# Optimization experiments

Hardware: AMD Instinct MI355X
Metric: run time of the kernel (lower is better)

The kernel has to match this reference:

```python
import jax, jax.numpy as jnp
import numpy as np

T, H_IN = 2048, 84
HID = 256
NA = 18


def _conv(x, w, b, stride):
    # x: [N,C,H,W], w: [O,I,kh,kw]
    y = jax.lax.conv_general_dilated(
        x, w, window_strides=(stride, stride), padding='VALID',
        dimension_numbers=('NCHW', 'OIHW', 'NCHW'))
    return jax.nn.relu(y + b[None, :, None, None])


def setup_inputs() -> dict:
    key = jax.random.key(0)
    ks = jax.random.split(key, 17)
    p = lambda k, shape, s=0.05: (jax.random.normal(k, shape, jnp.float32) * s)
    return {
        'input_frames': jax.random.uniform(ks[0], (T, 1, H_IN, H_IN), jnp.float32),
        'conv1_w': p(ks[1], (32, 1, 8, 8)),   'conv1_b': p(ks[2], (32,)),
        'conv2_w': p(ks[3], (64, 32, 4, 4)),  'conv2_b': p(ks[4], (64,)),
        'conv3_w': p(ks[5], (256, 64, 3, 3)), 'conv3_b': p(ks[6], (256,)),
        'attn_w1': p(ks[7], (HID, HID)),      'attn_b1': p(ks[8], (HID,)),
        'attn_w2': p(ks[9], (HID, HID)),      'attn_b2': p(ks[10], (HID,)),
        'lstm_w_ih': p(ks[11], (4 * HID, HID)), 'lstm_w_hh': p(ks[12], (4 * HID, HID)),
        'lstm_b_ih': p(ks[13], (4 * HID,)),     'lstm_b_hh': p(ks[14], (4 * HID,)),
        'q_w': p(ks[15], (NA, HID)),          'q_b': p(ks[16], (NA,)),
    }


def reference(input_frames, conv1_w, conv1_b, conv2_w, conv2_b, conv3_w, conv3_b,
              attn_w1, attn_b1, attn_w2, attn_b2,
              lstm_w_ih, lstm_w_hh, lstm_b_ih, lstm_b_hh, q_w, q_b):
    # CNN over all frames at once (loop in torch was over frames; math identical)
    x = _conv(input_frames, conv1_w, conv1_b, 4)   # [T,32,20,20]
    x = _conv(x, conv2_w, conv2_b, 2)              # [T,64,9,9]
    fm = _conv(x, conv3_w, conv3_b, 1)             # [T,256,7,7]
    t, c, hh, ww = fm.shape
    # build_vector: vectors[i, ch] = fm[ch, y, x], i = y*W + x
    vecs = fm.reshape(t, c, hh * ww).transpose(0, 2, 1)  # [T,49,256]

    def step(carry, v):
        h, cc = carry  # [256], [256]
        # additive attention; softmax over the 256 feature dim per spatial vector
        s = jnp.tanh(v @ attn_w1.T + attn_b1 + h)              # [49,256]
        w = jax.nn.softmax(s @ attn_w2.T + attn_b2, axis=-1)   # [49,256]
        ctx = jnp.sum(w * v, axis=0)                           # [256]
        # single-layer LSTM cell, torch gate order i,f,g,o
        gates = ctx @ lstm_w_ih.T + lstm_b_ih + h @ lstm_w_hh.T + lstm_b_hh
        i, f, g, o = jnp.split(gates, 4)
        c_new = jax.nn.sigmoid(f) * cc + jax.nn.sigmoid(i) * jnp.tanh(g)
        h_new = jax.nn.sigmoid(o) * jnp.tanh(c_new)
        return (h_new, c_new), None

    h0 = jnp.zeros((HID,), fm.dtype)
    (h_T, _), _ = jax.lax.scan(step, (h0, h0), vecs)
    q = h_T @ q_w.T + q_b          # [18]
    return q[None, :]              # [1, nr_actions], matches torch output
```

## Files before the change

kernel.cpp:

```cpp
#include <hip/hip_runtime.h>
#include <hip/hip_bf16.h>
#include <math.h>


#define T_FRAMES 2048
#define NI 49
#define HID 256
#define NA 18
#define NWG 8

typedef __bf16 v8bf __attribute__((ext_vector_type(8)));
typedef float v4f __attribute__((ext_vector_type(4)));

static constexpr size_t OFF_FM1   = 0;
static constexpr size_t OFF_FM2   = 104857600;
static constexpr size_t OFF_VECS  = 147324928;
static constexpr size_t OFF_W2B   = 250085376;
static constexpr size_t OFF_WIHB  = OFF_W2B  + 131072;
static constexpr size_t OFF_WHHB  = OFF_WIHB + 524288;
static constexpr size_t OFF_W1T   = OFF_WHHB + 524288;
static constexpr size_t OFF_HBUF  = OFF_FM2;
static constexpr size_t OFF_CPUB  = OFF_FM2 + 1024;
static constexpr size_t OFF_FLH   = OFF_FM2 + 9216;
static constexpr size_t OFF_FLC   = OFF_FM2 + 10240;

__global__ void prep_weights(const float* __restrict__ w2, const float* __restrict__ wih,
                             const float* __restrict__ whh, const float* __restrict__ w1,
                             __bf16* w2b, __bf16* wihb, __bf16* whhb, float* w1t) {
  int idx = blockIdx.x * 256 + threadIdx.x;
  int stride = gridDim.x * 256;
  for (int i = idx; i < 65536; i += stride) w2b[i] = (__bf16)w2[i];
  for (int i = idx; i < 262144; i += stride) wihb[i] = (__bf16)wih[i];
  for (int i = idx; i < 262144; i += stride) whhb[i] = (__bf16)whh[i];
  for (int i = idx; i < 65536; i += stride) {
    int r = i >> 8, c = i & 255;
    w1t[c * 256 + r] = w1[i];
  }
}

__global__ void conv1_k(const float* __restrict__ x, const float* __restrict__ w,
                        const float* __restrict__ b, float* __restrict__ y) {
  int idx = blockIdx.x * 256 + threadIdx.x;
  if (idx >= T_FRAMES * 32 * 20 * 20) return;
  int xx = idx % 20, yy = (idx / 20) % 20, o = (idx / 400) % 32, t = idx / 12800;
  const float* xp = x + t * 7056 + yy * 4 * 84 + xx * 4;
  const float* wp = w + o * 64;
  float acc = b[o];
  #pragma unroll
  for (int ky = 0; ky < 8; ky++)
    #pragma unroll
    for (int kx = 0; kx < 8; kx++)
      acc += xp[ky * 84 + kx] * wp[ky * 8 + kx];
  y[idx] = fmaxf(acc, 0.f);
}

__global__ __launch_bounds__(256) void conv2_k(const float* __restrict__ fm1, const float* __restrict__ w,
                                               const float* __restrict__ b, float* __restrict__ fm2) {
  __shared__ float xs[32 * 400];
  int t = blockIdx.x, tid = threadIdx.x;
  for (int i = tid; i < 12800; i += 256) xs[i] = fm1[t * 12800 + i];
  __syncthreads();
  int o = tid >> 2, q = tid & 3;
  int p0 = q * 21, p1 = (p0 + 21 < 81) ? p0 + 21 : 81;
  int ob[21];
  #pragma unroll
  for (int i2 = 0; i2 < 21; i2++) {
    int p = p0 + i2; if (p > 80) p = 80;
    int yy = p / 9, xx2 = p - yy * 9;
    ob[i2] = yy * 40 + xx2 * 2;
  }
  float acc[21];
  #pragma unroll
  for (int i2 = 0; i2 < 21; i2++) acc[i2] = 0.f;
  for (int c = 0; c < 32; c++) {
    int cbase = c * 400;
    for (int ky = 0; ky < 4; ky++)
      for (int kx = 0; kx < 4; kx++) {
        float wgt = w[((o * 32 + c) * 4 + ky) * 4 + kx];
        int kyo = ky * 20 + kx;
        #pragma unroll
        for (int i2 = 0; i2 < 21; i2++)
          acc[i2] += wgt * xs[cbase + ob[i2] + kyo];
      }
  }
  float bo = b[o];
  #pragma unroll
  for (int i2 = 0; i2 < 21; i2++) {
    int p = p0 + i2;
    if (p < p1) fm2[t * 5184 + o * 81 + p] = fmaxf(acc[i2] + bo, 0.f);
  }
}

__global__ __launch_bounds__(256) void conv3_k(const float* __restrict__ fm2, const float* __restrict__ w,
                                               const float* __restrict__ b, float* __restrict__ vecs) {
  __shared__ float xs[64 * 81];
  __shared__ float ws4[256][37];
  int t = blockIdx.x, tid = threadIdx.x;
  for (int i = tid; i < 64 * 81; i += 256) xs[i] = fm2[t * 5184 + i];
  float acc[49];
  #pragma unroll
  for (int i = 0; i < 49; i++) acc[i] = 0.f;
  for (int c0 = 0; c0 < 64; c0 += 4) {
    __syncthreads();
    for (int i = tid; i < 256 * 36; i += 256) {
      int oo = i / 36, j = i - oo * 36;
      ws4[oo][j] = w[oo * 576 + c0 * 9 + j];
    }
    __syncthreads();
    for (int cc = 0; cc < 4; cc++)
      for (int ky = 0; ky < 3; ky++)
        for (int kx = 0; kx < 3; kx++) {
          float wgt = ws4[tid][cc * 9 + ky * 3 + kx];
          const float* xp = &xs[(c0 + cc) * 81 + ky * 9 + kx];
          #pragma unroll
          for (int yy = 0; yy < 7; yy++)
            #pragma unroll
            for (int xx = 0; xx < 7; xx++)
              acc[yy * 7 + xx] += wgt * xp[yy * 9 + xx];
        }
  }
  float bo = b[tid];
  for (int i = 0; i < 49; i++)
    vecs[(t * 49 + i) * 256 + tid] = fmaxf(acc[i] + bo, 0.f);
}

__global__ __launch_bounds__(256) void aprep_k(const float* __restrict__ vecs, const float* __restrict__ w1t,
                                               const float* __restrict__ b1, float* __restrict__ A) {
  __shared__ float vs[49][256];
  int t = blockIdx.x, tid = threadIdx.x;
  for (int i = tid; i < 49 * 256; i += 256) vs[i >> 8][i & 255] = vecs[t * 12544 + i];
  __syncthreads();
  float acc[49];
  #pragma unroll
  for (int i = 0; i < 49; i++) acc[i] = 0.f;
  for (int k = 0; k < 256; k++) {
    float wgt = w1t[k * 256 + tid];
    #pragma unroll
    for (int i = 0; i < 49; i++) acc[i] += vs[i][k] * wgt;
  }
  float bb = b1[tid];
  for (int i = 0; i < 49; i++) A[(t * 49 + i) * 256 + tid] = acc[i] + bb;
}

__global__ void init_comm(unsigned* flh, unsigned* flc) {
  int idx = blockIdx.x * 512 + threadIdx.x;
  if (idx < NWG * 32) { flh[idx] = 0u; flc[idx] = 0u; }
}

__device__ __forceinline__ float tanh_fast(float x) {
  float e = __expf(2.f * x);
  return 1.f - 2.f / (e + 1.f);
}

__global__ __launch_bounds__(256, 1) void scan_k(
    const float* __restrict__ A, const float* __restrict__ vecs,
    const __bf16* __restrict__ w2b, const __bf16* __restrict__ wihb, const __bf16* __restrict__ whhb,
    const float* __restrict__ b2g, const float* __restrict__ bihg, const float* __restrict__ bhhg,
    const float* __restrict__ qw, const float* __restrict__ qb,
    float* hbuf, unsigned* cpub, unsigned* flh, unsigned* flc, float* out) {
  __shared__ __bf16 Ss[16][264];
  __shared__ float hs[HID];
  __shared__ __bf16 hbf[HID];
  __shared__ float Wt[8][HID];
  __shared__ float cxp[8][HID];
  __shared__ float b2s[HID];
  __shared__ float gb[4][32];

  const int w = blockIdx.x;
  const int tid = threadIdx.x;
  const int lane = tid & 63;
  const int wv = tid >> 6;
  const int quad = lane >> 4;
  const int l15 = lane & 15;
  const int r0 = 6 * w;
  const int nr = (w < 7) ? 6 : 7;
  const int prow = tid >> 5;
  const int pcol = (tid & 31) * 8;

  for (int i = tid; i < 16 * 264; i += 256) (&Ss[0][0])[i] = (__bf16)0.f;
  for (int i = tid; i < 8 * HID; i += 256) (&cxp[0][0])[i] = 0.f;
  b2s[tid] = b2g[tid];
  hs[tid] = 0.f;
  hbf[tid] = (__bf16)0.f;
  float cbias[4];
  if (tid < 32) {
    #pragma unroll
    for (int g = 0; g < 4; g++) {
      int row = 256 * g + 32 * w + tid;
      cbias[g] = bihg[row] + bhhg[row];
    }
  }
  float creg = 0.f;

  v8bf BW2[4][8];
  #pragma unroll
  for (int ntl = 0; ntl < 4; ntl++) {
    const int row = wv * 64 + ntl * 16 + l15;
    #pragma unroll
    for (int k = 0; k < 8; k++)
      BW2[ntl][k] = *(const v8bf*)(w2b + row * 256 + k * 32 + quad * 8);
  }
  v8bf BIH[2][8], BHH[2][8];
  #pragma unroll
  for (int nt = 0; nt < 2; nt++) {
    const int row = 256 * wv + 32 * w + nt * 16 + l15;
    #pragma unroll
    for (int k = 0; k < 8; k++) {
      BIH[nt][k] = *(const v8bf*)(wihb + row * 256 + k * 32 + quad * 8);
      BHH[nt][k] = *(const v8bf*)(whhb + row * 256 + k * 32 + quad * 8);
    }
  }
  __syncthreads();

  for (int t = 0; t < T_FRAMES; t++) {
    int rr = r0 + prow; if (rr > 48) rr = 48;
    const float* Ap = A + ((long)t * NI + rr) * HID + pcol;
    const float* Vp = vecs + ((long)t * NI + rr) * HID + pcol;
    const float4 a40 = *(const float4*)(Ap);
    const float4 a41 = *(const float4*)(Ap + 4);
    const float4 v40 = *(const float4*)(Vp);
    const float4 v41 = *(const float4*)(Vp + 4);

    if (t > 0) {
      if (wv == 0) {
        const unsigned tgt = (unsigned)t;
        int guard = 0;
        while (true) {
          unsigned fv = (lane < NWG)
              ? __hip_atomic_load(&flh[lane * 32], __ATOMIC_RELAXED, __HIP_MEMORY_SCOPE_AGENT)
              : tgt;
          if (__all(fv >= tgt) || ++guard > 5000000) break;
          __builtin_amdgcn_s_sleep(1);
        }
      }
      __syncthreads();
      float hv = __hip_atomic_load(&hbuf[tid], __ATOMIC_RELAXED, __HIP_MEMORY_SCOPE_AGENT);
      hs[tid] = hv;
      hbf[tid] = (__bf16)hv;
      __syncthreads();
    }

    if (prow < nr) {
      const float* hp = &hs[pcol];
      v8bf sv;
      sv[0] = (__bf16)tanh_fast(a40.x + hp[0]);
      sv[1] = (__bf16)tanh_fast(a40.y + hp[1]);
      sv[2] = (__bf16)tanh_fast(a40.z + hp[2]);
      sv[3] = (__bf16)tanh_fast(a40.w + hp[3]);
      sv[4] = (__bf16)tanh_fast(a41.x + hp[4]);
      sv[5] = (__bf16)tanh_fast(a41.y + hp[5]);
      sv[6] = (__bf16)tanh_fast(a41.z + hp[6]);
      sv[7] = (__bf16)tanh_fast(a41.w + hp[7]);
      *(v8bf*)&Ss[prow][pcol] = sv;
    }
    __syncthreads();

    v4f acc[4];
    #pragma unroll
    for (int ntl = 0; ntl < 4; ntl++) acc[ntl] = (v4f){0.f, 0.f, 0.f, 0.f};
    #pragma unroll
    for (int k = 0; k < 8; k++) {
      const v8bf av = *(const v8bf*)&Ss[l15][k * 32 + quad * 8];
      #pragma unroll
      for (int ntl = 0; ntl < 4; ntl++)
        acc[ntl] = __builtin_amdgcn_mfma_f32_16x16x32_bf16(av, BW2[ntl][k], acc[ntl], 0, 0, 0);
    }
    if (quad < 2) {
      #pragma unroll
      for (int ntl = 0; ntl < 4; ntl++) {
        const int col = wv * 64 + ntl * 16 + l15;
        const float bb = b2s[col];
        #pragma unroll
        for (int reg = 0; reg < 4; reg++)
          Wt[quad * 4 + reg][col] = acc[ntl][reg] + bb;
      }
    }
    __syncthreads();

    if (prow < nr) {
      float x[8];
      *(float4*)&x[0] = *(const float4*)&Wt[prow][pcol];
      *(float4*)&x[4] = *(const float4*)&Wt[prow][pcol + 4];
      float m = x[0];
      #pragma unroll
      for (int i = 1; i < 8; i++) m = fmaxf(m, x[i]);
      #pragma unroll
      for (int off = 16; off; off >>= 1) m = fmaxf(m, __shfl_xor(m, off, 64));
      float e[8], sm = 0.f;
      #pragma unroll
      for (int i = 0; i < 8; i++) { e[i] = __expf(x[i] - m); sm += e[i]; }
      #pragma unroll
      for (int off = 16; off; off >>= 1) sm += __shfl_xor(sm, off, 64);
      const float inv = 1.f / sm;
      cxp[prow][pcol + 0] = e[0] * inv * v40.x;
      cxp[prow][pcol + 1] = e[1] * inv * v40.y;
      cxp[prow][pcol + 2] = e[2] * inv * v40.z;
      cxp[prow][pcol + 3] = e[3] * inv * v40.w;
      cxp[prow][pcol + 4] = e[4] * inv * v41.x;
      cxp[prow][pcol + 5] = e[5] * inv * v41.y;
      cxp[prow][pcol + 6] = e[6] * inv * v41.z;
      cxp[prow][pcol + 7] = e[7] * inv * v41.w;
    }
    __syncthreads();

    float cp = 0.f;
    #pragma unroll
    for (int r = 0; r < 8; r++) cp += cxp[r][tid];
    float cpo = __shfl_xor(cp, 1, 64);
    if ((tid & 1) == 0) {
      union { __bf16 b; unsigned short s; } lo, hi;
      lo.b = (__bf16)cp; hi.b = (__bf16)cpo;
      unsigned u = ((unsigned)hi.s << 16) | (unsigned)lo.s;
      __hip_atomic_store(&cpub[w * 256 + (tid >> 1)], u, __ATOMIC_RELAXED, __HIP_MEMORY_SCOPE_AGENT);
    }
    __syncthreads();
    if (tid == 0)
      __hip_atomic_store(&flc[w * 32], (unsigned)(t + 1), __ATOMIC_RELEASE, __HIP_MEMORY_SCOPE_AGENT);

    v4f gacc[2];
    gacc[0] = (v4f){0.f, 0.f, 0.f, 0.f};
    gacc[1] = (v4f){0.f, 0.f, 0.f, 0.f};
    #pragma unroll
    for (int k = 0; k < 8; k++) {
      v8bf hf;
      #pragma unroll
      for (int z = 0; z < 8; z++) hf[z] = (__bf16)0.f;
      if (l15 == 0) hf = *(const v8bf*)&hbf[k * 32 + quad * 8];
      gacc[0] = __builtin_amdgcn_mfma_f32_16x16x32_bf16(hf, BHH[0][k], gacc[0], 0, 0, 0);
      gacc[1] = __builtin_amdgcn_mfma_f32_16x16x32_bf16(hf, BHH[1][k], gacc[1], 0, 0, 0);
    }

    {
      const unsigned tgt = (unsigned)(t + 1);
      int guard = 0;
      while (true) {
        unsigned fv = (lane < NWG)
            ? __hip_atomic_load(&flc[lane * 32], __ATOMIC_RELAXED, __HIP_MEMORY_SCOPE_AGENT)
            : tgt;
        if (__all(fv >= tgt) || ++guard > 5000000) break;
        __builtin_amdgcn_s_sleep(1);
      }
    }

    #pragma unroll
    for (int k = 0; k < 8; k++) {
      union { unsigned long long u[2]; v8bf v; } pf;
      pf.u[0] = 0ull; pf.u[1] = 0ull;
      if (l15 < NWG) {
        const unsigned long long* src =
            (const unsigned long long*)(cpub + l15 * 256) + (k * 8 + quad * 2);
        pf.u[0] = __hip_atomic_load(src, __ATOMIC_RELAXED, __HIP_MEMORY_SCOPE_AGENT);
        pf.u[1] = __hip_atomic_load(src + 1, __ATOMIC_RELAXED, __HIP_MEMORY_SCOPE_AGENT);
      }
      gacc[0] = __builtin_amdgcn_mfma_f32_16x16x32_bf16(pf.v, BIH[0][k], gacc[0], 0, 0, 0);
      gacc[1] = __builtin_amdgcn_mfma_f32_16x16x32_bf16(pf.v, BIH[1][k], gacc[1], 0, 0, 0);
    }
    #pragma unroll
    for (int nt = 0; nt < 2; nt++) {
      float tot = gacc[nt][0] + gacc[nt][1] + gacc[nt][2] + gacc[nt][3];
      tot += __shfl_xor(tot, 16, 64);
      tot += __shfl_xor(tot, 32, 64);
      if (lane < 16) gb[wv][nt * 16 + lane] = tot;
    }
    __syncthreads();

    if (tid < 32) {
      float gi = gb[0][tid] + cbias[0];
      float gf = gb[1][tid] + cbias[1];
      float gg = gb[2][tid] + cbias[2];
      float go = gb[3][tid] + cbias[3];
      float si = 1.f / (1.f + __expf(-gi));
      float sf = 1.f / (1.f + __expf(-gf));
      float so = 1.f / (1.f + __expf(-go));
      creg = sf * creg + si * tanh_fast(gg);
      float hn = so * tanh_fast(creg);
      __hip_atomic_store(&hbuf[32 * w + tid], hn, __ATOMIC_RELAXED, __HIP_MEMORY_SCOPE_AGENT);
    }
    __syncthreads();
    if (tid == 0)
      __hip_atomic_store(&flh[w * 32], (unsigned)(t + 1), __ATOMIC_RELEASE, __HIP_MEMORY_SCOPE_AGENT);
  }

  if (w == 0) {
    if (wv == 0) {
      const unsigned tgt = (unsigned)T_FRAMES;
      int guard = 0;
      while (true) {
        unsigned fv = (lane < NWG)
            ? __hip_atomic_load(&flh[lane * 32], __ATOMIC_RELAXED, __HIP_MEMORY_SCOPE_AGENT)
            : tgt;
        if (__all(fv >= tgt) || ++guard > 5000000) break;
        __builtin_amdgcn_s_sleep(1);
      }
    }
    __syncthreads();
    hs[tid] = __hip_atomic_load(&hbuf[tid], __ATOMIC_RELAXED, __HIP_MEMORY_SCOPE_AGENT);
    __syncthreads();
    if (tid < NA) {
      float acc = qb[tid];
      for (int k = 0; k < HID; k++) acc += hs[k] * qw[tid * HID + k];
      out[tid] = acc;
    }
  }
}

extern "C" void kernel_launch(void* const* d_in, const int* in_sizes, int n_in,
                              void* d_out, int out_size, void* d_ws, size_t ws_size,
                              hipStream_t stream) {
  const float* frames = (const float*)d_in[0];
  const float* c1w = (const float*)d_in[1];
  const float* c1b = (const float*)d_in[2];
  const float* c2w = (const float*)d_in[3];
  const float* c2b = (const float*)d_in[4];
  const float* c3w = (const float*)d_in[5];
  const float* c3b = (const float*)d_in[6];
  const float* aw1 = (const float*)d_in[7];
  const float* ab1 = (const float*)d_in[8];
  const float* aw2 = (const float*)d_in[9];
  const float* ab2 = (const float*)d_in[10];
  const float* wih = (const float*)d_in[11];
  const float* whh = (const float*)d_in[12];
  const float* bih = (const float*)d_in[13];
  const float* bhh = (const float*)d_in[14];
  const float* qw  = (const float*)d_in[15];
  const float* qb  = (const float*)d_in[16];

  char* ws = (char*)d_ws;
  float*  fm1   = (float*)(ws + OFF_FM1);
  float*  A     = (float*)(ws + OFF_FM1);
  float*  fm2   = (float*)(ws + OFF_FM2);
  float*  vecs  = (float*)(ws + OFF_VECS);
  __bf16* w2b   = (__bf16*)(ws + OFF_W2B);
  __bf16* wihb  = (__bf16*)(ws + OFF_WIHB);
  __bf16* whhb  = (__bf16*)(ws + OFF_WHHB);
  float*  w1t   = (float*)(ws + OFF_W1T);
  float*    hbuf = (float*)(ws + OFF_HBUF);
  unsigned* cpub = (unsigned*)(ws + OFF_CPUB);
  unsigned* flh  = (unsigned*)(ws + OFF_FLH);
  unsigned* flc  = (unsigned*)(ws + OFF_FLC);

  prep_weights<<<256, 256, 0, stream>>>(aw2, wih, whh, aw1, w2b, wihb, whhb, w1t);
  conv1_k<<<102400, 256, 0, stream>>>(frames, c1w, c1b, fm1);
  conv2_k<<<T_FRAMES, 256, 0, stream>>>(fm1, c2w, c2b, fm2);
  conv3_k<<<T_FRAMES, 256, 0, stream>>>(fm2, c3w, c3b, vecs);
  aprep_k<<<T_FRAMES, 256, 0, stream>>>(vecs, w1t, ab1, A);
  init_comm<<<1, 512, 0, stream>>>(flh, flc);
  scan_k<<<NWG, 256, 0, stream>>>(A, vecs, w2b, wihb, whhb, ab2, bih, bhh, qw, qb,
                                  hbuf, cpub, flh, flc, (float*)d_out);
}
```

Baseline: 16.00 ms.

## Replace flag-based cross-workgroup sync with sequence-tagged 64-bit data packets

Each published h value and context pair is packed together with its step counter into one 64-bit word. Consumers poll the data itself until every tag matches, instead of waiting on separate release/acquire flags and then loading. This removes the flag stores, the extra __syncthreads around publishing, and a serial flag-then-data round trip on every LSTM step. In exchange every thread polls several words (32 per lane for the context), which adds L2 traffic and spin pressure, and the poll loop drops the s_sleep backoff.

```diff
diff --git a/kernel.cpp b/kernel.cpp
--- a/kernel.cpp
+++ b/kernel.cpp
@@ -8,9 +8,11 @@
 #define HID 256
 #define NA 18
 #define NWG 8
+#define POLL_MAX 1000000
 
 typedef __bf16 v8bf __attribute__((ext_vector_type(8)));
 typedef float v4f __attribute__((ext_vector_type(4)));
+typedef unsigned long long u64;
 
 static constexpr size_t OFF_FM1   = 0;
 static constexpr size_t OFF_FM2   = 104857600;
@@ -19,10 +21,15 @@
 static constexpr size_t OFF_WIHB  = OFF_W2B  + 131072;
 static constexpr size_t OFF_WHHB  = OFF_WIHB + 524288;
 static constexpr size_t OFF_W1T   = OFF_WHHB + 524288;
-static constexpr size_t OFF_HBUF  = OFF_FM2;
-static constexpr size_t OFF_CPUB  = OFF_FM2 + 1024;
-static constexpr size_t OFF_FLH   = OFF_FM2 + 9216;
-static constexpr size_t OFF_FLC   = OFF_FM2 + 10240;
+static constexpr size_t OFF_HPUB  = OFF_FM2;
+static constexpr size_t OFF_CPUB  = OFF_FM2 + 2048;
+
+__device__ __forceinline__ u64 ld_pair(const u64* p) {
+  return __hip_atomic_load(p, __ATOMIC_RELAXED, __HIP_MEMORY_SCOPE_AGENT);
+}
+__device__ __forceinline__ void st_pair(u64* p, u64 v) {
+  __hip_atomic_store(p, v, __ATOMIC_RELAXED, __HIP_MEMORY_SCOPE_AGENT);
+}
 
 __global__ void prep_weights(const float* __restrict__ w2, const float* __restrict__ wih,
                              const float* __restrict__ whh, const float* __restrict__ w1,
@@ -142,9 +149,10 @@
   for (int i = 0; i < 49; i++) A[(t * 49 + i) * 256 + tid] = acc[i] + bb;
 }
 
-__global__ void init_comm(unsigned* flh, unsigned* flc) {
-  int idx = blockIdx.x * 512 + threadIdx.x;
-  if (idx < NWG * 32) { flh[idx] = 0u; flc[idx] = 0u; }
+__global__ void init_comm(u64* hpub, u64* cpub) {
+  int idx = blockIdx.x * 256 + threadIdx.x;
+  if (idx < 256) hpub[idx] = 0ull;
+  if (idx < NWG * 128) cpub[idx] = 0ull;
 }
 
 __device__ __forceinline__ float tanh_fast(float x) {
@@ -157,14 +165,14 @@
     const __bf16* __restrict__ w2b, const __bf16* __restrict__ wihb, const __bf16* __restrict__ whhb,
     const float* __restrict__ b2g, const float* __restrict__ bihg, const float* __restrict__ bhhg,
     const float* __restrict__ qw, const float* __restrict__ qb,
-    float* hbuf, unsigned* cpub, unsigned* flh, unsigned* flc, float* out) {
+    u64* hpub, u64* cpub, float* out) {
   __shared__ __bf16 Ss[16][264];
-  __shared__ float hs[HID];
   __shared__ __bf16 hbf[HID];
   __shared__ float Wt[8][HID];
   __shared__ float cxp[8][HID];
   __shared__ float b2s[HID];
   __shared__ float gb[4][32];
+  __shared__ float hsf[HID];
 
   const int w = blockIdx.x;
   const int tid = threadIdx.x;
@@ -176,11 +184,11 @@
   const int nr = (w < 7) ? 6 : 7;
   const int prow = tid >> 5;
   const int pcol = (tid & 31) * 8;
+  int dead = 0;
 
   for (int i = tid; i < 16 * 264; i += 256) (&Ss[0][0])[i] = (__bf16)0.f;
   for (int i = tid; i < 8 * HID; i += 256) (&cxp[0][0])[i] = 0.f;
   b2s[tid] = b2g[tid];
-  hs[tid] = 0.f;
   hbf[tid] = (__bf16)0.f;
   float cbias[4];
   if (tid < 32) {
@@ -221,36 +229,42 @@
     const float4 v40 = *(const float4*)(Vp);
     const float4 v41 = *(const float4*)(Vp + 4);
 
+    float hreg[8];
+    #pragma unroll
+    for (int i = 0; i < 8; i++) hreg[i] = 0.f;
     if (t > 0) {
-      if (wv == 0) {
-        const unsigned tgt = (unsigned)t;
-        int guard = 0;
-        while (true) {
-          unsigned fv = (lane < NWG)
-              ? __hip_atomic_load(&flh[lane * 32], __ATOMIC_RELAXED, __HIP_MEMORY_SCOPE_AGENT)
-              : tgt;
-          if (__all(fv >= tgt) || ++guard > 5000000) break;
-          __builtin_amdgcn_s_sleep(1);
+      const unsigned tgt = (unsigned)t;
+      const u64* hp = hpub + pcol;
+      u64 v[8], vo = 0;
+      #pragma unroll
+      for (int i = 0; i < 8; i++) v[i] = 0;
+      if (!dead) {
+        for (int guard = 0;; ++guard) {
+          #pragma unroll
+          for (int i = 0; i < 8; i++) v[i] = ld_pair(hp + i);
+          vo = ld_pair(hpub + tid);
+          unsigned ok = (unsigned)(vo >> 32) == tgt;
+          #pragma unroll
+          for (int i = 0; i < 8; i++) ok &= ((unsigned)(v[i] >> 32) == tgt);
+          if (__all(ok)) break;
+          if (guard >= POLL_MAX) { dead = 1; break; }
         }
       }
-      __syncthreads();
-      float hv = __hip_atomic_load(&hbuf[tid], __ATOMIC_RELAXED, __HIP_MEMORY_SCOPE_AGENT);
-      hs[tid] = hv;
-      hbf[tid] = (__bf16)hv;
-      __syncthreads();
+      #pragma unroll
+      for (int i = 0; i < 8; i++) hreg[i] = __uint_as_float((unsigned)v[i]);
+      hbf[tid] = (__bf16)__uint_as_float((unsigned)vo);
     }
 
     if (prow < nr) {
-      const float* hp = &hs[pcol];
       v8bf sv;
-      sv[0] = (__bf16)tanh_fast(a40.x + hp[0]);
-      sv[1] = (__bf16)tanh_fast(a40.y + hp[1]);
-      sv[2] = (__bf16)tanh_fast(a40.z + hp[2]);
-      sv[3] = (__bf16)tanh_fast(a40.w + hp[3]);
-      sv[4] = (__bf16)tanh_fast(a41.x + hp[4]);
-      sv[5] = (__bf16)tanh_fast(a41.y + hp[5]);
-      sv[6] = (__bf16)tanh_fast(a41.z + hp[6]);
-      sv[7] = (__bf16)tanh_fast(a41.w + hp[7]);
+      sv[0] = (__bf16)tanh_fast(a40.x + hreg[0]);
+      sv[1] = (__bf16)tanh_fast(a40.y + hreg[1]);
+      sv[2] = (__bf16)tanh_fast(a40.z + hreg[2]);
+      sv[3] = (__bf16)tanh_fast(a40.w + hreg[3]);
+      sv[4] = (__bf16)tanh_fast(a41.x + hreg[4]);
+      sv[5] = (__bf16)tanh_fast(a41.y + hreg[5]);
+      sv[6] = (__bf16)tanh_fast(a41.z + hreg[6]);
+      sv[7] = (__bf16)tanh_fast(a41.w + hreg[7]);
       *(v8bf*)&Ss[prow][pcol] = sv;
     }
     __syncthreads();
@@ -310,12 +324,10 @@
     if ((tid & 1) == 0) {
       union { __bf16 b; unsigned short s; } lo, hi;
       lo.b = (__bf16)cp; hi.b = (__bf16)cpo;
-      unsigned u = ((unsigned)hi.s << 16) | (unsigned)lo.s;
-      __hip_atomic_store(&cpub[w * 256 + (tid >> 1)], u, __ATOMIC_RELAXED, __HIP_MEMORY_SCOPE_AGENT);
-    }
-    __syncthreads();
-    if (tid == 0)
-      __hip_atomic_store(&flc[w * 32], (unsigned)(t + 1), __ATOMIC_RELEASE, __HIP_MEMORY_SCOPE_AGENT);
+      unsigned dat = ((unsigned)hi.s << 16) | (unsigned)lo.s;
+      u64 pv = ((u64)(unsigned)(t + 1) << 32) | (u64)dat;
+      st_pair(&cpub[w * 128 + (tid >> 1)], pv);
+    }
 
     v4f gacc[2];
     gacc[0] = (v4f){0.f, 0.f, 0.f, 0.f};
@@ -331,29 +343,35 @@
     }
 
     {
-      const unsigned tgt = (unsigned)(t + 1);
-      int guard = 0;
-      while (true) {
-        unsigned fv = (lane < NWG)
-            ? __hip_atomic_load(&flc[lane * 32], __ATOMIC_RELAXED, __HIP_MEMORY_SCOPE_AGENT)
-            : tgt;
-        if (__all(fv >= tgt) || ++guard > 5000000) break;
-        __builtin_amdgcn_s_sleep(1);
-      }
-    }
-
-    #pragma unroll
-    for (int k = 0; k < 8; k++) {
-      union { unsigned long long u[2]; v8bf v; } pf;
-      pf.u[0] = 0ull; pf.u[1] = 0ull;
-      if (l15 < NWG) {
-        const unsigned long long* src =
-            (const unsigned long long*)(cpub + l15 * 256) + (k * 8 + quad * 2);
-        pf.u[0] = __hip_atomic_load(src, __ATOMIC_RELAXED, __HIP_MEMORY_SCOPE_AGENT);
-        pf.u[1] = __hip_atomic_load(src + 1, __ATOMIC_RELAXED, __HIP_MEMORY_SCOPE_AGENT);
-      }
-      gacc[0] = __builtin_amdgcn_mfma_f32_16x16x32_bf16(pf.v, BIH[0][k], gacc[0], 0, 0, 0);
-      gacc[1] = __builtin_amdgcn_mfma_f32_16x16x32_bf16(pf.v, BIH[1][k], gacc[1], 0, 0, 0);
+      const unsigned tgt2 = (unsigned)(t + 1);
+      const u64* cb = cpub + (l15 & 7) * 128 + quad * 4;
+      u64 cv[32];
+      #pragma unroll
+      for (int i = 0; i < 32; i++) cv[i] = 0;
+      if (!dead) {
+        for (int guard = 0;; ++guard) {
+          #pragma unroll
+          for (int k = 0; k < 8; k++)
+            #pragma unroll
+            for (int i = 0; i < 4; i++)
+              cv[k * 4 + i] = ld_pair(cb + k * 16 + i);
+          unsigned ok = 1;
+          #pragma unroll
+          for (int i = 0; i < 32; i++) ok &= ((unsigned)(cv[i] >> 32) == tgt2);
+          if (__all(ok)) break;
+          if (guard >= POLL_MAX) { dead = 1; break; }
+        }
+      }
+      const bool zrow = (l15 >= 8);
+      #pragma unroll
+      for (int k = 0; k < 8; k++) {
+        union { unsigned u[4]; v8bf v; } pf;
+        #pragma unroll
+        for (int i = 0; i < 4; i++)
+          pf.u[i] = zrow ? 0u : (unsigned)cv[k * 4 + i];
+        gacc[0] = __builtin_amdgcn_mfma_f32_16x16x32_bf16(pf.v, BIH[0][k], gacc[0], 0, 0, 0);
+        gacc[1] = __builtin_amdgcn_mfma_f32_16x16x32_bf16(pf.v, BIH[1][k], gacc[1], 0, 0, 0);
+      }
     }
     #pragma unroll
     for (int nt = 0; nt < 2; nt++) {
@@ -374,31 +392,26 @@
       float so = 1.f / (1.f + __expf(-go));
       creg = sf * creg + si * tanh_fast(gg);
       float hn = so * tanh_fast(creg);
-      __hip_atomic_store(&hbuf[32 * w + tid], hn, __ATOMIC_RELAXED, __HIP_MEMORY_SCOPE_AGENT);
-    }
-    __syncthreads();
-    if (tid == 0)
-      __hip_atomic_store(&flh[w * 32], (unsigned)(t + 1), __ATOMIC_RELEASE, __HIP_MEMORY_SCOPE_AGENT);
+      u64 pv = ((u64)(unsigned)(t + 1) << 32) | (u64)__float_as_uint(hn);
+      st_pair(&hpub[32 * w + tid], pv);
+    }
   }
 
   if (w == 0) {
-    if (wv == 0) {
-      const unsigned tgt = (unsigned)T_FRAMES;
-      int guard = 0;
-      while (true) {
-        unsigned fv = (lane < NWG)
-            ? __hip_atomic_load(&flh[lane * 32], __ATOMIC_RELAXED, __HIP_MEMORY_SCOPE_AGENT)
-            : tgt;
-        if (__all(fv >= tgt) || ++guard > 5000000) break;
-        __builtin_amdgcn_s_sleep(1);
-      }
-    }
-    __syncthreads();
-    hs[tid] = __hip_atomic_load(&hbuf[tid], __ATOMIC_RELAXED, __HIP_MEMORY_SCOPE_AGENT);
+    const unsigned tgt = (unsigned)T_FRAMES;
+    u64 vo = 0;
+    if (!dead) {
+      for (int guard = 0;; ++guard) {
+        vo = ld_pair(hpub + tid);
+        if (__all((unsigned)(vo >> 32) == tgt)) break;
+        if (guard >= POLL_MAX) { dead = 1; break; }
+      }
+    }
+    hsf[tid] = __uint_as_float((unsigned)vo);
     __syncthreads();
     if (tid < NA) {
       float acc = qb[tid];
-      for (int k = 0; k < HID; k++) acc += hs[k] * qw[tid * HID + k];
+      for (int k = 0; k < HID; k++) acc += hsf[k] * qw[tid * HID + k];
       out[tid] = acc;
     }
   }
@@ -434,17 +447,15 @@
   __bf16* wihb  = (__bf16*)(ws + OFF_WIHB);
   __bf16* whhb  = (__bf16*)(ws + OFF_WHHB);
   float*  w1t   = (float*)(ws + OFF_W1T);
-  float*    hbuf = (float*)(ws + OFF_HBUF);
-  unsigned* cpub = (unsigned*)(ws + OFF_CPUB);
-  unsigned* flh  = (unsigned*)(ws + OFF_FLH);
-  unsigned* flc  = (unsigned*)(ws + OFF_FLC);
+  u64* hpub = (u64*)(ws + OFF_HPUB);
+  u64* cpub = (u64*)(ws + OFF_CPUB);
 
   prep_weights<<<256, 256, 0, stream>>>(aw2, wih, whh, aw1, w2b, wihb, whhb, w1t);
   conv1_k<<<102400, 256, 0, stream>>>(frames, c1w, c1b, fm1);
   conv2_k<<<T_FRAMES, 256, 0, stream>>>(fm1, c2w, c2b, fm2);
   conv3_k<<<T_FRAMES, 256, 0, stream>>>(fm2, c3w, c3b, vecs);
   aprep_k<<<T_FRAMES, 256, 0, stream>>>(vecs, w1t, ab1, A);
-  init_comm<<<1, 512, 0, stream>>>(flh, flc);
+  init_comm<<<4, 256, 0, stream>>>(hpub, cpub);
   scan_k<<<NWG, 256, 0, stream>>>(A, vecs, w2b, wihb, whhb, ab2, bih, bhh, qw, qb,
-                                  hbuf, cpub, flh, flc, (float*)d_out);
-}
+                                  hpub, cpub, (float*)d_out);
+}
```

Result: slower. 19.96 ms (+24.7%).

## Compute full attention context redundantly per workgroup to drop one cross-WG barrier

Applied to the files above, without the earlier changes.

Each of the 8 scan workgroups now processes all 49 spatial vectors itself (4 M-tiles of MFMA plus a softmax over every row), instead of splitting the rows across workgroups and exchanging partial contexts through global memory with a second flag barrier. This removes one inter-workgroup handshake per timestep from the serial recurrence. The attention precompute A and the vectors are stored in bf16 to halve the per-step global reads. Spin waits drop the sleep and use acquire loads. The cost is 8x redundant attention work per step and some extra bf16 rounding.

```diff
diff --git a/kernel.cpp b/kernel.cpp
--- a/kernel.cpp
+++ b/kernel.cpp
@@ -8,10 +8,13 @@
 #define HID 256
 #define NA 18
 #define NWG 8
+#define POLL_MAX 2000000
 
 typedef __bf16 v8bf __attribute__((ext_vector_type(8)));
 typedef float v4f __attribute__((ext_vector_type(4)));
 
+static constexpr size_t OFF_ABF   = 0;
+static constexpr size_t OFF_VBF   = 51380224;
 static constexpr size_t OFF_FM1   = 0;
 static constexpr size_t OFF_FM2   = 104857600;
 static constexpr size_t OFF_VECS  = 147324928;
@@ -20,9 +23,7 @@
 static constexpr size_t OFF_WHHB  = OFF_WIHB + 524288;
 static constexpr size_t OFF_W1T   = OFF_WHHB + 524288;
 static constexpr size_t OFF_HBUF  = OFF_FM2;
-static constexpr size_t OFF_CPUB  = OFF_FM2 + 1024;
-static constexpr size_t OFF_FLH   = OFF_FM2 + 9216;
-static constexpr size_t OFF_FLC   = OFF_FM2 + 10240;
+static constexpr size_t OFF_FLH   = OFF_FM2 + 1024;
 
 __global__ void prep_weights(const float* __restrict__ w2, const float* __restrict__ wih,
                              const float* __restrict__ whh, const float* __restrict__ w1,
@@ -92,7 +93,8 @@
 }
 
 __global__ __launch_bounds__(256) void conv3_k(const float* __restrict__ fm2, const float* __restrict__ w,
-                                               const float* __restrict__ b, float* __restrict__ vecs) {
+                                               const float* __restrict__ b, float* __restrict__ vecs,
+                                               __bf16* __restrict__ vb) {
   __shared__ float xs[64 * 81];
   __shared__ float ws4[256][37];
   int t = blockIdx.x, tid = threadIdx.x;
@@ -120,12 +122,15 @@
         }
   }
   float bo = b[tid];
-  for (int i = 0; i < 49; i++)
-    vecs[(t * 49 + i) * 256 + tid] = fmaxf(acc[i] + bo, 0.f);
+  for (int i = 0; i < 49; i++) {
+    float val = fmaxf(acc[i] + bo, 0.f);
+    vecs[(t * 49 + i) * 256 + tid] = val;
+    vb[(t * 49 + i) * 256 + tid] = (__bf16)val;
+  }
 }
 
 __global__ __launch_bounds__(256) void aprep_k(const float* __restrict__ vecs, const float* __restrict__ w1t,
-                                               const float* __restrict__ b1, float* __restrict__ A) {
+                                               const float* __restrict__ b1, __bf16* __restrict__ Ab) {
   __shared__ float vs[49][256];
   int t = blockIdx.x, tid = threadIdx.x;
   for (int i = tid; i < 49 * 256; i += 256) vs[i >> 8][i & 255] = vecs[t * 12544 + i];
@@ -139,12 +144,12 @@
     for (int i = 0; i < 49; i++) acc[i] += vs[i][k] * wgt;
   }
   float bb = b1[tid];
-  for (int i = 0; i < 49; i++) A[(t * 49 + i) * 256 + tid] = acc[i] + bb;
-}
-
-__global__ void init_comm(unsigned* flh, unsigned* flc) {
-  int idx = blockIdx.x * 512 + threadIdx.x;
-  if (idx < NWG * 32) { flh[idx] = 0u; flc[idx] = 0u; }
+  for (int i = 0; i < 49; i++) Ab[(t * 49 + i) * 256 + tid] = (__bf16)(acc[i] + bb);
+}
+
+__global__ void init_comm(unsigned* flh) {
+  int idx = threadIdx.x;
+  if (idx < NWG * 32) flh[idx] = 0u;
 }
 
 __device__ __forceinline__ float tanh_fast(float x) {
@@ -153,16 +158,18 @@
 }
 
 __global__ __launch_bounds__(256, 1) void scan_k(
-    const float* __restrict__ A, const float* __restrict__ vecs,
+    const __bf16* __restrict__ Abf, const __bf16* __restrict__ vbf,
     const __bf16* __restrict__ w2b, const __bf16* __restrict__ wihb, const __bf16* __restrict__ whhb,
     const float* __restrict__ b2g, const float* __restrict__ bihg, const float* __restrict__ bhhg,
     const float* __restrict__ qw, const float* __restrict__ qb,
-    float* hbuf, unsigned* cpub, unsigned* flh, unsigned* flc, float* out) {
-  __shared__ __bf16 Ss[16][264];
+    float* hbuf, unsigned* flh, float* out) {
+  __shared__ __attribute__((aligned(16))) __bf16 Ss[64][264];
+  __shared__ __attribute__((aligned(16))) __bf16 Vs[49][264];
+  __shared__ float Wt[49][257];
+  __shared__ float ctxp[4][256];
   __shared__ float hs[HID];
-  __shared__ __bf16 hbf[HID];
-  __shared__ float Wt[8][HID];
-  __shared__ float cxp[8][HID];
+  __shared__ __attribute__((aligned(16))) __bf16 hbf[HID];
+  __shared__ __attribute__((aligned(16))) __bf16 cxbf[HID];
   __shared__ float b2s[HID];
   __shared__ float gb[4][32];
 
@@ -172,13 +179,11 @@
   const int wv = tid >> 6;
   const int quad = lane >> 4;
   const int l15 = lane & 15;
-  const int r0 = 6 * w;
-  const int nr = (w < 7) ? 6 : 7;
-  const int prow = tid >> 5;
-  const int pcol = (tid & 31) * 8;
-
-  for (int i = tid; i < 16 * 264; i += 256) (&Ss[0][0])[i] = (__bf16)0.f;
-  for (int i = tid; i < 8 * HID; i += 256) (&cxp[0][0])[i] = 0.f;
+  const int r8 = tid >> 5;
+  const int c32 = tid & 31;
+  int dead = 0;
+
+  for (int i = tid; i < 64 * 264; i += 256) (&Ss[0][0])[i] = (__bf16)0.f;
   b2s[tid] = b2g[tid];
   hs[tid] = 0.f;
   hbf[tid] = (__bf16)0.f;
@@ -213,24 +218,25 @@
   __syncthreads();
 
   for (int t = 0; t < T_FRAMES; t++) {
-    int rr = r0 + prow; if (rr > 48) rr = 48;
-    const float* Ap = A + ((long)t * NI + rr) * HID + pcol;
-    const float* Vp = vecs + ((long)t * NI + rr) * HID + pcol;
-    const float4 a40 = *(const float4*)(Ap);
-    const float4 a41 = *(const float4*)(Ap + 4);
-    const float4 v40 = *(const float4*)(Vp);
-    const float4 v41 = *(const float4*)(Vp + 4);
+    v8bf aR[7], vR[7];
+    #pragma unroll
+    for (int rr = 0; rr < 7; rr++) {
+      int i = r8 * 7 + rr;
+      long off = ((long)t * NI + ((i < NI) ? i : NI - 1)) * HID + c32 * 8;
+      aR[rr] = *(const v8bf*)(Abf + off);
+      vR[rr] = *(const v8bf*)(vbf + off);
+    }
 
     if (t > 0) {
-      if (wv == 0) {
+      if (wv == 0 && !dead) {
         const unsigned tgt = (unsigned)t;
         int guard = 0;
         while (true) {
           unsigned fv = (lane < NWG)
-              ? __hip_atomic_load(&flh[lane * 32], __ATOMIC_RELAXED, __HIP_MEMORY_SCOPE_AGENT)
+              ? __hip_atomic_load(&flh[lane * 32], __ATOMIC_ACQUIRE, __HIP_MEMORY_SCOPE_AGENT)
               : tgt;
-          if (__all(fv >= tgt) || ++guard > 5000000) break;
-          __builtin_amdgcn_s_sleep(1);
+          if (__all(fv >= tgt)) break;
+          if (++guard > POLL_MAX) { dead = 1; break; }
         }
       }
       __syncthreads();
@@ -240,120 +246,102 @@
       __syncthreads();
     }
 
-    if (prow < nr) {
-      const float* hp = &hs[pcol];
-      v8bf sv;
-      sv[0] = (__bf16)tanh_fast(a40.x + hp[0]);
-      sv[1] = (__bf16)tanh_fast(a40.y + hp[1]);
-      sv[2] = (__bf16)tanh_fast(a40.z + hp[2]);
-      sv[3] = (__bf16)tanh_fast(a40.w + hp[3]);
-      sv[4] = (__bf16)tanh_fast(a41.x + hp[4]);
-      sv[5] = (__bf16)tanh_fast(a41.y + hp[5]);
-      sv[6] = (__bf16)tanh_fast(a41.z + hp[6]);
-      sv[7] = (__bf16)tanh_fast(a41.w + hp[7]);
-      *(v8bf*)&Ss[prow][pcol] = sv;
-    }
-    __syncthreads();
-
-    v4f acc[4];
-    #pragma unroll
-    for (int ntl = 0; ntl < 4; ntl++) acc[ntl] = (v4f){0.f, 0.f, 0.f, 0.f};
+    {
+      float hr[8];
+      #pragma unroll
+      for (int e = 0; e < 8; e++) hr[e] = hs[c32 * 8 + e];
+      #pragma unroll
+      for (int rr = 0; rr < 7; rr++) {
+        int i = r8 * 7 + rr;
+        if (i < NI) {
+          v8bf sv;
+          #pragma unroll
+          for (int e = 0; e < 8; e++)
+            sv[e] = (__bf16)tanh_fast((float)aR[rr][e] + hr[e]);
+          *(v8bf*)&Ss[i][c32 * 8] = sv;
+          *(v8bf*)&Vs[i][c32 * 8] = vR[rr];
+        }
+      }
+    }
+    __syncthreads();
+
+    v4f acc[4][4];
+    #pragma unroll
+    for (int mt = 0; mt < 4; mt++)
+      #pragma unroll
+      for (int ntl = 0; ntl < 4; ntl++) acc[mt][ntl] = (v4f){0.f, 0.f, 0.f, 0.f};
     #pragma unroll
     for (int k = 0; k < 8; k++) {
-      const v8bf av = *(const v8bf*)&Ss[l15][k * 32 + quad * 8];
-      #pragma unroll
-      for (int ntl = 0; ntl < 4; ntl++)
-        acc[ntl] = __builtin_amdgcn_mfma_f32_16x16x32_bf16(av, BW2[ntl][k], acc[ntl], 0, 0, 0);
-    }
-    if (quad < 2) {
+      v8bf av[4];
+      #pragma unroll
+      for (int mt = 0; mt < 4; mt++)
+        av[mt] = *(const v8bf*)&Ss[mt * 16 + l15][k * 32 + quad * 8];
+      #pragma unroll
+      for (int mt = 0; mt < 4; mt++)
+        #pragma unroll
+        for (int ntl = 0; ntl < 4; ntl++)
+          acc[mt][ntl] = __builtin_amdgcn_mfma_f32_16x16x32_bf16(av[mt], BW2[ntl][k], acc[mt][ntl], 0, 0, 0);
+    }
+    #pragma unroll
+    for (int mt = 0; mt < 4; mt++)
       #pragma unroll
       for (int ntl = 0; ntl < 4; ntl++) {
         const int col = wv * 64 + ntl * 16 + l15;
         const float bb = b2s[col];
         #pragma unroll
-        for (int reg = 0; reg < 4; reg++)
-          Wt[quad * 4 + reg][col] = acc[ntl][reg] + bb;
-      }
-    }
-    __syncthreads();
-
-    if (prow < nr) {
-      float x[8];
-      *(float4*)&x[0] = *(const float4*)&Wt[prow][pcol];
-      *(float4*)&x[4] = *(const float4*)&Wt[prow][pcol + 4];
-      float m = x[0];
-      #pragma unroll
-      for (int i = 1; i < 8; i++) m = fmaxf(m, x[i]);
-      #pragma unroll
-      for (int off = 16; off; off >>= 1) m = fmaxf(m, __shfl_xor(m, off, 64));
-      float e[8], sm = 0.f;
-      #pragma unroll
-      for (int i = 0; i < 8; i++) { e[i] = __expf(x[i] - m); sm += e[i]; }
-      #pragma unroll
-      for (int off = 16; off; off >>= 1) sm += __shfl_xor(sm, off, 64);
-      const float inv = 1.f / sm;
-      cxp[prow][pcol + 0] = e[0] * inv * v40.x;
-      cxp[prow][pcol + 1] = e[1] * inv * v40.y;
-      cxp[prow][pcol + 2] = e[2] * inv * v40.z;
-      cxp[prow][pcol + 3] = e[3] * inv * v40.w;
-      cxp[prow][pcol + 4] = e[4] * inv * v41.x;
-      cxp[prow][pcol + 5] = e[5] * inv * v41.y;
-      cxp[prow][pcol + 6] = e[6] * inv * v41.z;
-      cxp[prow][pcol + 7] = e[7] * inv * v41.w;
-    }
-    __syncthreads();
-
-    float cp = 0.f;
-    #pragma unroll
-    for (int r = 0; r < 8; r++) cp += cxp[r][tid];
-    float cpo = __shfl_xor(cp, 1, 64);
-    if ((tid & 1) == 0) {
-      union { __bf16 b; unsigned short s; } lo, hi;
-      lo.b = (__bf16)cp; hi.b = (__bf16)cpo;
-      unsigned u = ((unsigned)hi.s << 16) | (unsigned)lo.s;
-      __hip_atomic_store(&cpub[w * 256 + (tid >> 1)], u, __ATOMIC_RELAXED, __HIP_MEMORY_SCOPE_AGENT);
-    }
-    __syncthreads();
-    if (tid == 0)
-      __hip_atomic_store(&flc[w * 32], (unsigned)(t + 1), __ATOMIC_RELEASE, __HIP_MEMORY_SCOPE_AGENT);
+        for (int reg = 0; reg < 4; reg++) {
+          int grow = mt * 16 + quad * 4 + reg;
+          if (grow < NI) Wt[grow][col] = acc[mt][ntl][reg] + bb;
+        }
+      }
+    __syncthreads();
+
+    {
+      float cacc[4] = {0.f, 0.f, 0.f, 0.f};
+      for (int i = wv; i < NI; i += 4) {
+        float x[4];
+        #pragma unroll
+        for (int j = 0; j < 4; j++) x[j] = Wt[i][lane + 64 * j];
+        float m = fmaxf(fmaxf(x[0], x[1]), fmaxf(x[2], x[3]));
+        #pragma unroll
+        for (int off = 32; off; off >>= 1) m = fmaxf(m, __shfl_xor(m, off, 64));
+        float e[4], sm = 0.f;
+        #pragma unroll
+        for (int j = 0; j < 4; j++) { e[j] = __expf(x[j] - m); sm += e[j]; }
+        #pragma unroll
+        for (int off = 32; off; off >>= 1) sm += __shfl_xor(sm, off, 64);
+        const float inv = 1.f / sm;
+        #pragma unroll
+        for (int j = 0; j < 4; j++)
+          cacc[j] += e[j] * inv * (float)Vs[i][lane + 64 * j];
+      }
+      #pragma unroll
+      for (int j = 0; j < 4; j++) ctxp[wv][lane + 64 * j] = cacc[j];
+    }
+    __syncthreads();
+
+    {
+      float cx = ctxp[0][tid] + ctxp[1][tid] + ctxp[2][tid] + ctxp[3][tid];
+      cxbf[tid] = (__bf16)cx;
+    }
+    __syncthreads();
 
     v4f gacc[2];
     gacc[0] = (v4f){0.f, 0.f, 0.f, 0.f};
     gacc[1] = (v4f){0.f, 0.f, 0.f, 0.f};
     #pragma unroll
     for (int k = 0; k < 8; k++) {
-      v8bf hf;
-      #pragma unroll
-      for (int z = 0; z < 8; z++) hf[z] = (__bf16)0.f;
-      if (l15 == 0) hf = *(const v8bf*)&hbf[k * 32 + quad * 8];
+      v8bf cf, hf;
+      #pragma unroll
+      for (int z = 0; z < 8; z++) { cf[z] = (__bf16)0.f; hf[z] = (__bf16)0.f; }
+      if (l15 == 0) {
+        cf = *(const v8bf*)&cxbf[k * 32 + quad * 8];
+        hf = *(const v8bf*)&hbf[k * 32 + quad * 8];
+      }
+      gacc[0] = __builtin_amdgcn_mfma_f32_16x16x32_bf16(cf, BIH[0][k], gacc[0], 0, 0, 0);
       gacc[0] = __builtin_amdgcn_mfma_f32_16x16x32_bf16(hf, BHH[0][k], gacc[0], 0, 0, 0);
+      gacc[1] = __builtin_amdgcn_mfma_f32_16x16x32_bf16(cf, BIH[1][k], gacc[1], 0, 0, 0);
       gacc[1] = __builtin_amdgcn_mfma_f32_16x16x32_bf16(hf, BHH[1][k], gacc[1], 0, 0, 0);
-    }
-
-    {
-      const unsigned tgt = (unsigned)(t + 1);
-      int guard = 0;
-      while (true) {
-        unsigned fv = (lane < NWG)
-            ? __hip_atomic_load(&flc[lane * 32], __ATOMIC_RELAXED, __HIP_MEMORY_SCOPE_AGENT)
-            : tgt;
-        if (__all(fv >= tgt) || ++guard > 5000000) break;
-        __builtin_amdgcn_s_sleep(1);
-      }
-    }
-
-    #pragma unroll
-    for (int k = 0; k < 8; k++) {
-      union { unsigned long long u[2]; v8bf v; } pf;
-      pf.u[0] = 0ull; pf.u[1] = 0ull;
-      if (l15 < NWG) {
-        const unsigned long long* src =
-            (const unsigned long long*)(cpub + l15 * 256) + (k * 8 + quad * 2);
-        pf.u[0] = __hip_atomic_load(src, __ATOMIC_RELAXED, __HIP_MEMORY_SCOPE_AGENT);
-        pf.u[1] = __hip_atomic_load(src + 1, __ATOMIC_RELAXED, __HIP_MEMORY_SCOPE_AGENT);
-      }
-      gacc[0] = __builtin_amdgcn_mfma_f32_16x16x32_bf16(pf.v, BIH[0][k], gacc[0], 0, 0, 0);
-      gacc[1] = __builtin_amdgcn_mfma_f32_16x16x32_bf16(pf.v, BIH[1][k], gacc[1], 0, 0, 0);
     }
     #pragma unroll
     for (int nt = 0; nt < 2; nt++) {
@@ -382,15 +370,15 @@
   }
 
   if (w == 0) {
-    if (wv == 0) {
+    if (wv == 0 && !dead) {
       const unsigned tgt = (unsigned)T_FRAMES;
       int guard = 0;
       while (true) {
         unsigned fv = (lane < NWG)
-            ? __hip_atomic_load(&flh[lane * 32], __ATOMIC_RELAXED, __HIP_MEMORY_SCOPE_AGENT)
+            ? __hip_atomic_load(&flh[lane * 32], __ATOMIC_ACQUIRE, __HIP_MEMORY_SCOPE_AGENT)
             : tgt;
-        if (__all(fv >= tgt) || ++guard > 5000000) break;
-        __builtin_amdgcn_s_sleep(1);
+        if (__all(fv >= tgt)) break;
+        if (++guard > POLL_MAX) { dead = 1; break; }
       }
     }
     __syncthreads();
@@ -427,7 +415,8 @@
 
   char* ws = (char*)d_ws;
   float*  fm1   = (float*)(ws + OFF_FM1);
-  float*  A     = (float*)(ws + OFF_FM1);
+  __bf16* Abf   = (__bf16*)(ws + OFF_ABF);
+  __bf16* vbf   = (__bf16*)(ws + OFF_VBF);
   float*  fm2   = (float*)(ws + OFF_FM2);
   float*  vecs  = (float*)(ws + OFF_VECS);
   __bf16* w2b   = (__bf16*)(ws + OFF_W2B);
@@ -435,16 +424,14 @@
   __bf16* whhb  = (__bf16*)(ws + OFF_WHHB);
   float*  w1t   = (float*)(ws + OFF_W1T);
   float*    hbuf = (float*)(ws + OFF_HBUF);
-  unsigned* cpub = (unsigned*)(ws + OFF_CPUB);
   unsigned* flh  = (unsigned*)(ws + OFF_FLH);
-  unsigned* flc  = (unsigned*)(ws + OFF_FLC);
 
   prep_weights<<<256, 256, 0, stream>>>(aw2, wih, whh, aw1, w2b, wihb, whhb, w1t);
   conv1_k<<<102400, 256, 0, stream>>>(frames, c1w, c1b, fm1);
   conv2_k<<<T_FRAMES, 256, 0, stream>>>(fm1, c2w, c2b, fm2);
-  conv3_k<<<T_FRAMES, 256, 0, stream>>>(fm2, c3w, c3b, vecs);
-  aprep_k<<<T_FRAMES, 256, 0, stream>>>(vecs, w1t, ab1, A);
-  init_comm<<<1, 512, 0, stream>>>(flh, flc);
-  scan_k<<<NWG, 256, 0, stream>>>(A, vecs, w2b, wihb, whhb, ab2, bih, bhh, qw, qb,
-                                  hbuf, cpub, flh, flc, (float*)d_out);
-}
+  conv3_k<<<T_FRAMES, 256, 0, stream>>>(fm2, c3w, c3b, vecs, vbf);
+  aprep_k<<<T_FRAMES, 256, 0, stream>>>(vecs, w1t, ab1, Abf);
+  init_comm<<<1, 256, 0, stream>>>(flh);
+  scan_k<<<NWG, 256, 0, stream>>>(Abf, vbf, w2b, wihb, whhb, ab2, bih, bhh, qw, qb,
+                                  hbuf, flh, (float*)d_out);
+}
```

Result: slower. 32.40 ms (+102.5%).
